# Kernel optimization log

Hardware: AMD Instinct MI355X
Metric: run time of the kernel (lower is better)

The kernel has to match this reference:

```python
import jax, jax.numpy as jnp
import numpy as np

B, C, H, W = 32, 64, 64, 64   # C == embedding_dim
K = 1024                      # num_embeddings


def setup_inputs() -> dict:
    key = jax.random.key(0)
    kx, ke = jax.random.split(key)
    x = jax.random.normal(kx, (B, C, H, W), dtype=jnp.float32)
    # codebook init in torch is uniform(-sqrt(3), sqrt(3)); any float values work for the math
    limit = 3.0 ** 0.5
    embedding = jax.random.uniform(ke, (K, C), dtype=jnp.float32, minval=-limit, maxval=limit)
    return {"x": x, "embedding": embedding}


def reference(x, embedding):
    """Eval-mode forward of Vector_Quantizer (EMA buffer updates are a
    training-only in-place side effect and are not part of the functional output)."""
    Bx, Cx, Hx, Wx = x.shape
    # [B, C, H, W] -> [B*H*W, C]
    flat_x = jnp.transpose(x, (0, 2, 3, 1)).reshape(-1, Cx)
    # squared L2 distances: ||z||^2 - 2 z.e^T + ||e||^2   -> [N, K]
    distances = (
        jnp.sum(flat_x * flat_x, axis=1, keepdims=True)
        - 2.0 * (flat_x @ embedding.T)
        + jnp.sum(embedding * embedding, axis=1)[None, :]
    )
    encoding_indices = jnp.argmin(distances, axis=1)            # [N] int
    quantized = embedding[encoding_indices]                     # [N, C] gather
    quantized = quantized.reshape(Bx, Hx, Wx, Cx).transpose(0, 3, 1, 2)  # [B,C,H,W]
    # commitment loss: 0.25 * mse(stop_grad(quantized), x)
    e_latent_loss = jnp.mean((jax.lax.stop_gradient(quantized) - x) ** 2)
    loss = 0.25 * e_latent_loss
    # straight-through estimator
    quantized_st = x + jax.lax.stop_gradient(quantized - x)
    return loss, quantized_st, encoding_indices
```

## Files before the change

kernel.cpp:

```cpp
#include <hip/hip_runtime.h>

#define NPTS   131072
#define CDIM   64
#define KCODES 1024
#define HW     4096
#define CHW    (CDIM*HW)
#define NELEM  8388608

#define FLAG_THR 2.5e-2f
#define WLCAP    32768
#define NFB_WAVES 1024

typedef __attribute__((ext_vector_type(8))) short bf16x8;
typedef __attribute__((ext_vector_type(4))) float f32x4;

#define WS_NORM_OFF 8
#define WS_EHI_OFF  (8 + KCODES)

__device__ inline unsigned short f32_to_bf16_rn(float f) {
    unsigned u = __builtin_bit_cast(unsigned, f);
    unsigned r = (u + 0x7FFFu + ((u >> 16) & 1u)) >> 16;
    return (unsigned short)r;
}
__device__ inline float bf16_to_f32(unsigned short h) {
    unsigned u = ((unsigned)h) << 16;
    return __builtin_bit_cast(float, u);
}

__global__ void vq_prep(const float* __restrict__ emb, float* __restrict__ ws) {
    int k = blockIdx.x * 256 + threadIdx.x;
    float* norms = ws + WS_NORM_OFF;
    unsigned short* ehi = (unsigned short*)(ws + WS_EHI_OFF);
    unsigned short* elo = ehi + KCODES * CDIM;
    int* wl_cnt = (int*)(elo + KCODES * CDIM);
    if (k == 0) { ws[0] = 0.0f; *wl_cnt = 0; }
    if (k < KCODES) {
        const float4* row = (const float4*)(emb + k * CDIM);
        double s = 0.0;
        #pragma unroll
        for (int c4 = 0; c4 < CDIM / 4; ++c4) {
            float4 v = row[c4];
            s += (double)v.x * v.x + (double)v.y * v.y
               + (double)v.z * v.z + (double)v.w * v.w;
            float vv[4] = {v.x, v.y, v.z, v.w};
            #pragma unroll
            for (int t = 0; t < 4; ++t) {
                unsigned short hi = f32_to_bf16_rn(vv[t]);
                float hif = bf16_to_f32(hi);
                unsigned short lo = f32_to_bf16_rn(vv[t] - hif);
                ehi[k * CDIM + c4 * 4 + t] = hi;
                elo[k * CDIM + c4 * 4 + t] = lo;
            }
        }
        norms[k] = (float)s;
    }
}

__global__ __launch_bounds__(256) void vq_main(
    const float* __restrict__ x,
    const float* __restrict__ emb,
    float* __restrict__ ws,
    float* __restrict__ out)
{
    const float* norms = ws + WS_NORM_OFF;
    const unsigned short* ehi = (const unsigned short*)(ws + WS_EHI_OFF);
    const unsigned short* elo = ehi + KCODES * CDIM;
    int* wl_cnt = (int*)(elo + KCODES * CDIM);
    int* wl = wl_cnt + 16;

    const int lane = threadIdx.x & 63;
    const int widx = threadIdx.x >> 6;
    const int wb   = (blockIdx.x * 4 + widx) * 64;
    const int lrow = lane & 15;
    const int lk   = lane >> 4;

    __shared__ int   s_idx[4][64];
    __shared__ float s_gap[4][64];

    bf16x8 ahi[4][2], alo[4][2];
    #pragma unroll
    for (int m = 0; m < 4; ++m) {
        int p = wb + m * 16 + lrow;
        const float* xb = x + (p >> 12) * CHW + (p & (HW - 1));
        #pragma unroll
        for (int h = 0; h < 2; ++h) {
            #pragma unroll
            for (int j = 0; j < 8; ++j) {
                int c = h * 32 + lk * 8 + j;
                float v = -2.0f * xb[c * HW];
                unsigned short hi = f32_to_bf16_rn(v);
                float hif = bf16_to_f32(hi);
                unsigned short lo = f32_to_bf16_rn(v - hif);
                ahi[m][h][j] = (short)hi;
                alo[m][h][j] = (short)lo;
            }
        }
    }

    float best[4][4], sec[4][4];
    int   bidx[4][4];
    #pragma unroll
    for (int m = 0; m < 4; ++m)
        #pragma unroll
        for (int r = 0; r < 4; ++r) { best[m][r] = 3.4e38f; sec[m][r] = 3.4e38f; bidx[m][r] = 0; }

    for (int n0 = 0; n0 < KCODES; n0 += 16) {
        const int code = n0 + lrow;
        const unsigned short* eh = ehi + code * CDIM + lk * 8;
        const unsigned short* el = elo + code * CDIM + lk * 8;
        bf16x8 bh0 = *(const bf16x8*)(eh);
        bf16x8 bh1 = *(const bf16x8*)(eh + 32);
        bf16x8 bl0 = *(const bf16x8*)(el);
        bf16x8 bl1 = *(const bf16x8*)(el + 32);
        float nrm = norms[code];

        f32x4 acc[4];
        #pragma unroll
        for (int m = 0; m < 4; ++m) acc[m] = (f32x4){nrm, nrm, nrm, nrm};
        #pragma unroll
        for (int m = 0; m < 4; ++m) acc[m] = __builtin_amdgcn_mfma_f32_16x16x32_bf16(ahi[m][0], bh0, acc[m], 0, 0, 0);
        #pragma unroll
        for (int m = 0; m < 4; ++m) acc[m] = __builtin_amdgcn_mfma_f32_16x16x32_bf16(ahi[m][1], bh1, acc[m], 0, 0, 0);
        #pragma unroll
        for (int m = 0; m < 4; ++m) acc[m] = __builtin_amdgcn_mfma_f32_16x16x32_bf16(alo[m][0], bh0, acc[m], 0, 0, 0);
        #pragma unroll
        for (int m = 0; m < 4; ++m) acc[m] = __builtin_amdgcn_mfma_f32_16x16x32_bf16(alo[m][1], bh1, acc[m], 0, 0, 0);
        #pragma unroll
        for (int m = 0; m < 4; ++m) acc[m] = __builtin_amdgcn_mfma_f32_16x16x32_bf16(ahi[m][0], bl0, acc[m], 0, 0, 0);
        #pragma unroll
        for (int m = 0; m < 4; ++m) acc[m] = __builtin_amdgcn_mfma_f32_16x16x32_bf16(ahi[m][1], bl1, acc[m], 0, 0, 0);

        #pragma unroll
        for (int m = 0; m < 4; ++m) {
            #pragma unroll
            for (int r = 0; r < 4; ++r) {
                float sc = acc[m][r];
                bool  lt = sc < best[m][r];
                float ns = fminf(sec[m][r], sc);
                sec[m][r]  = lt ? best[m][r] : ns;
                best[m][r] = lt ? sc : best[m][r];
                bidx[m][r] = lt ? code : bidx[m][r];
            }
        }
    }

    #pragma unroll
    for (int m = 0; m < 4; ++m) {
        #pragma unroll
        for (int r = 0; r < 4; ++r) {
            float b_ = best[m][r], s_ = sec[m][r];
            int   i_ = bidx[m][r];
            #pragma unroll
            for (int msk = 1; msk < 16; msk <<= 1) {
                float ob = __shfl_xor(b_, msk, 64);
                float os = __shfl_xor(s_, msk, 64);
                int   oi = __shfl_xor(i_, msk, 64);
                float nsec = fminf(fminf(s_, os), fmaxf(b_, ob));
                bool take = (ob < b_) || (ob == b_ && oi < i_);
                b_ = take ? ob : b_;
                i_ = take ? oi : i_;
                s_ = nsec;
            }
            if (lrow == 0) {
                int pl = m * 16 + lk * 4 + r;
                s_idx[widx][pl] = i_;
                s_gap[widx][pl] = s_ - b_;
            }
        }
    }
    __syncthreads();

    const int p = wb + lane;
    const int myidx = s_idx[widx][lane];
    const float gap = s_gap[widx][lane];
    if (gap < FLAG_THR) {
        int slot = atomicAdd(wl_cnt, 1);
        if (slot < WLCAP) wl[slot] = p;
    }
    out[1 + NELEM + p] = (float)myidx;

    const int b = p >> 12, sp = p & (HW - 1);
    const float*  xr   = x + b * CHW + sp;
    float*        orow = out + 1 + b * CHW + sp;
    const float4* er   = (const float4*)(emb + myidx * CDIM);
    float lsum = 0.0f;
    #pragma unroll
    for (int c4 = 0; c4 < CDIM / 4; ++c4) {
        float4 q = er[c4];
        float qq[4] = {q.x, q.y, q.z, q.w};
        #pragma unroll
        for (int t = 0; t < 4; ++t) {
            int c = c4 * 4 + t;
            float xv = xr[c * HW];
            float d = qq[t] - xv;
            lsum += d * d;
            orow[c * HW] = qq[t];
        }
    }
    #pragma unroll
    for (int off = 32; off > 0; off >>= 1)
        lsum += __shfl_down(lsum, off, 64);
    if (lane == 0) atomicAdd(ws, lsum);
}

__global__ __launch_bounds__(256) void vq_fallback(
    const float* __restrict__ x,
    const float* __restrict__ emb,
    float* __restrict__ ws,
    float* __restrict__ out)
{
    const unsigned short* ehi = (const unsigned short*)(ws + WS_EHI_OFF);
    const unsigned short* elo = ehi + KCODES * CDIM;
    const int* wl_cnt = (const int*)(elo + KCODES * CDIM);
    const int* wl = wl_cnt + 16;

    const int lane = threadIdx.x & 63;
    const int slot = blockIdx.x * 4 + (threadIdx.x >> 6);
    int cnt = *wl_cnt;
    if (cnt > WLCAP) cnt = WLCAP;

    for (int i = slot; i < cnt; i += NFB_WAVES) {
        const int p = wl[i];
        const int b = p >> 12, sp = p & (HW - 1);
        const float* xr = x + b * CHW + sp;
        float z[CDIM];
        #pragma unroll
        for (int c = 0; c < CDIM; ++c) z[c] = xr[c * HW];

        double bd = 1e300;
        int    bi = 0;
        for (int kk = 0; kk < 16; ++kk) {
            int k = kk * 64 + lane;
            const float4* er = (const float4*)(emb + k * CDIM);
            double s = 0.0;
            #pragma unroll
            for (int c4 = 0; c4 < CDIM / 4; ++c4) {
                float4 e = er[c4];
                double t0 = (double)z[c4 * 4 + 0] - (double)e.x;
                double t1 = (double)z[c4 * 4 + 1] - (double)e.y;
                double t2 = (double)z[c4 * 4 + 2] - (double)e.z;
                double t3 = (double)z[c4 * 4 + 3] - (double)e.w;
                s += t0 * t0 + t1 * t1 + t2 * t2 + t3 * t3;
            }
            if (s < bd) { bd = s; bi = k; }
        }
        #pragma unroll
        for (int msk = 1; msk < 64; msk <<= 1) {
            double od = __shfl_xor(bd, msk, 64);
            int    oi = __shfl_xor(bi, msk, 64);
            bool take = (od < bd) || (od == bd && oi < bi);
            bd = take ? od : bd;
            bi = take ? oi : bi;
        }
        const int oldidx = (int)out[1 + NELEM + p];
        if (bi != oldidx) {
            if (lane == 0) out[1 + NELEM + p] = (float)bi;
            float xv = xr[lane * HW];
            float qn = emb[bi * CDIM + lane];
            float qo = emb[oldidx * CDIM + lane];
            out[1 + b * CHW + lane * HW + sp] = qn;
            float dl = (qn - xv) * (qn - xv) - (qo - xv) * (qo - xv);
            #pragma unroll
            for (int off = 32; off > 0; off >>= 1)
                dl += __shfl_down(dl, off, 64);
            if (lane == 0) atomicAdd(ws, dl);
        }
    }
}

__global__ void vq_final(const float* __restrict__ ws, float* __restrict__ out) {
    if (threadIdx.x == 0 && blockIdx.x == 0)
        out[0] = 0.25f * ws[0] / (float)NELEM;
}

extern "C" void kernel_launch(void* const* d_in, const int* in_sizes, int n_in,
                              void* d_out, int out_size, void* d_ws, size_t ws_size,
                              hipStream_t stream) {
    const float* x   = (const float*)d_in[0];
    const float* emb = (const float*)d_in[1];
    float* out = (float*)d_out;
    float* ws  = (float*)d_ws;

    vq_prep<<<4, 256, 0, stream>>>(emb, ws);
    vq_main<<<NPTS / 256, 256, 0, stream>>>(x, emb, ws, out);
    vq_fallback<<<NFB_WAVES / 4, 256, 0, stream>>>(x, emb, ws, out);
    vq_final<<<1, 64, 0, stream>>>(ws, out);
}
```

Baseline: 218.5 us.

## Switch distance GEMM to fp16 split, packed integer keys, and pre-swizzled codebook

Replaces the bf16 hi/lo six-MFMA scheme with an fp16 split of scaled x (four MFMAs per tile, codebook kept in fp16 only), and packs quantised distance plus code index into a 32-bit key so min3/med3 instructions track the best and second-best candidates. The codebook is pre-laid out in MFMA-fragment order with norms, and the loads are double-buffered across code groups. Near-ties are still sent to the exact fallback through an integer-gap threshold. This cuts MFMA count and argmin ALU work, but quantising distances to integer keys and dropping the codebook low part may send more points to the fallback path.

```diff
diff --git a/kernel.cpp b/kernel.cpp
--- a/kernel.cpp
+++ b/kernel.cpp
@@ -7,65 +7,51 @@
 #define CHW    (CDIM*HW)
 #define NELEM  8388608
 
-#define FLAG_THR 2.5e-2f
-#define WLCAP    32768
-#define NFB_WAVES 1024
-
-typedef __attribute__((ext_vector_type(8))) short bf16x8;
-typedef __attribute__((ext_vector_type(4))) float f32x4;
-
-#define WS_NORM_OFF 8
-#define WS_EHI_OFF  (8 + KCODES)
-
-__device__ inline unsigned short f32_to_bf16_rn(float f) {
-    unsigned u = __builtin_bit_cast(unsigned, f);
-    unsigned r = (u + 0x7FFFu + ((u >> 16) & 1u)) >> 16;
-    return (unsigned short)r;
-}
-__device__ inline float bf16_to_f32(unsigned short h) {
-    unsigned u = ((unsigned)h) << 16;
-    return __builtin_bit_cast(float, u);
+#define NGROUP  64
+#define GSTRIDE 2304
+#define WS_BP   8
+#define WS_WL   (WS_BP + (NGROUP*GSTRIDE)/4)
+#define WLCAP   16384
+#define NFB_WAVES 2048
+#define THR_KEY (256u << 10)
+
+typedef __attribute__((ext_vector_type(8))) _Float16 f16x8;
+typedef __attribute__((ext_vector_type(4))) float    f32x4;
+
+__device__ inline unsigned umin3(unsigned a, unsigned b, unsigned c) {
+    unsigned d; asm("v_min3_u32 %0, %1, %2, %3" : "=v"(d) : "v"(a), "v"(b), "v"(c)); return d;
+}
+__device__ inline unsigned umed3(unsigned a, unsigned b, unsigned c) {
+    unsigned d; asm("v_med3_u32 %0, %1, %2, %3" : "=v"(d) : "v"(a), "v"(b), "v"(c)); return d;
 }
 
 __global__ void vq_prep(const float* __restrict__ emb, float* __restrict__ ws) {
-    int k = blockIdx.x * 256 + threadIdx.x;
-    float* norms = ws + WS_NORM_OFF;
-    unsigned short* ehi = (unsigned short*)(ws + WS_EHI_OFF);
-    unsigned short* elo = ehi + KCODES * CDIM;
-    int* wl_cnt = (int*)(elo + KCODES * CDIM);
-    if (k == 0) { ws[0] = 0.0f; *wl_cnt = 0; }
-    if (k < KCODES) {
-        const float4* row = (const float4*)(emb + k * CDIM);
-        double s = 0.0;
-        #pragma unroll
-        for (int c4 = 0; c4 < CDIM / 4; ++c4) {
-            float4 v = row[c4];
-            s += (double)v.x * v.x + (double)v.y * v.y
-               + (double)v.z * v.z + (double)v.w * v.w;
-            float vv[4] = {v.x, v.y, v.z, v.w};
-            #pragma unroll
-            for (int t = 0; t < 4; ++t) {
-                unsigned short hi = f32_to_bf16_rn(vv[t]);
-                float hif = bf16_to_f32(hi);
-                unsigned short lo = f32_to_bf16_rn(vv[t] - hif);
-                ehi[k * CDIM + c4 * 4 + t] = hi;
-                elo[k * CDIM + c4 * 4 + t] = lo;
-            }
-        }
-        norms[k] = (float)s;
-    }
-}
-
-__global__ __launch_bounds__(256) void vq_main(
-    const float* __restrict__ x,
-    const float* __restrict__ emb,
-    float* __restrict__ ws,
-    float* __restrict__ out)
+    int t = blockIdx.x * 256 + threadIdx.x;
+    if (t == 0) { ws[0] = 0.0f; ((int*)(ws + WS_WL))[0] = 0; }
+    int g = t >> 6, l = t & 63;
+    int code = g * 16 + (l & 15);
+    int ch0  = (l >> 4) * 8;
+    char* bp = (char*)(ws + WS_BP) + g * GSTRIDE;
+    const float* row = emb + code * CDIM;
+    double s = 0.0;
+    for (int c = 0; c < CDIM; ++c) { double v = row[c]; s += v * v; }
+    *(float*)(bp + 2048 + l * 4) = (float)(s * 1024.0);
+    f16x8 h0, h1;
+    #pragma unroll
+    for (int j = 0; j < 8; ++j) {
+        h0[j] = (_Float16)row[ch0 + j];
+        h1[j] = (_Float16)row[32 + ch0 + j];
+    }
+    *(f16x8*)(bp + l * 16)        = h0;
+    *(f16x8*)(bp + 1024 + l * 16) = h1;
+}
+
+__global__ __launch_bounds__(256, 2) void vq_main(
+    const float* __restrict__ x, const float* __restrict__ emb,
+    float* __restrict__ ws, float* __restrict__ out)
 {
-    const float* norms = ws + WS_NORM_OFF;
-    const unsigned short* ehi = (const unsigned short*)(ws + WS_EHI_OFF);
-    const unsigned short* elo = ehi + KCODES * CDIM;
-    int* wl_cnt = (int*)(elo + KCODES * CDIM);
+    const char* bp = (const char*)(ws + WS_BP);
+    int* wl_cnt = (int*)(ws + WS_WL);
     int* wl = wl_cnt + 16;
 
     const int lane = threadIdx.x & 63;
@@ -74,96 +60,119 @@
     const int lrow = lane & 15;
     const int lk   = lane >> 4;
 
-    __shared__ int   s_idx[4][64];
-    __shared__ float s_gap[4][64];
-
-    bf16x8 ahi[4][2], alo[4][2];
+    __shared__ int      s_idx[4][64];
+    __shared__ unsigned s_gap[4][64];
+
+    f16x8 ah[4][2], al[4][2];
+    float znorm[4];
     #pragma unroll
     for (int m = 0; m < 4; ++m) {
         int p = wb + m * 16 + lrow;
         const float* xb = x + (p >> 12) * CHW + (p & (HW - 1));
+        float zsq = 0.f;
         #pragma unroll
         for (int h = 0; h < 2; ++h) {
             #pragma unroll
             for (int j = 0; j < 8; ++j) {
                 int c = h * 32 + lk * 8 + j;
-                float v = -2.0f * xb[c * HW];
-                unsigned short hi = f32_to_bf16_rn(v);
-                float hif = bf16_to_f32(hi);
-                unsigned short lo = f32_to_bf16_rn(v - hif);
-                ahi[m][h][j] = (short)hi;
-                alo[m][h][j] = (short)lo;
-            }
-        }
-    }
-
-    float best[4][4], sec[4][4];
-    int   bidx[4][4];
+                float v = -2048.0f * xb[c * HW];
+                zsq = fmaf(v, v, zsq);
+                _Float16 hi = (_Float16)v;
+                _Float16 lo = (_Float16)(v - (float)hi);
+                ah[m][h][j] = hi; al[m][h][j] = lo;
+            }
+        }
+        zsq *= (1.0f / 4096.0f);
+        zsq += __shfl_xor(zsq, 16, 64);
+        zsq += __shfl_xor(zsq, 32, 64);
+        znorm[m] = zsq;
+    }
+    f32x4 zs[4];
     #pragma unroll
     for (int m = 0; m < 4; ++m)
         #pragma unroll
-        for (int r = 0; r < 4; ++r) { best[m][r] = 3.4e38f; sec[m][r] = 3.4e38f; bidx[m][r] = 0; }
-
-    for (int n0 = 0; n0 < KCODES; n0 += 16) {
-        const int code = n0 + lrow;
-        const unsigned short* eh = ehi + code * CDIM + lk * 8;
-        const unsigned short* el = elo + code * CDIM + lk * 8;
-        bf16x8 bh0 = *(const bf16x8*)(eh);
-        bf16x8 bh1 = *(const bf16x8*)(eh + 32);
-        bf16x8 bl0 = *(const bf16x8*)(el);
-        bf16x8 bl1 = *(const bf16x8*)(el + 32);
-        float nrm = norms[code];
-
-        f32x4 acc[4];
-        #pragma unroll
-        for (int m = 0; m < 4; ++m) acc[m] = (f32x4){nrm, nrm, nrm, nrm};
-        #pragma unroll
-        for (int m = 0; m < 4; ++m) acc[m] = __builtin_amdgcn_mfma_f32_16x16x32_bf16(ahi[m][0], bh0, acc[m], 0, 0, 0);
-        #pragma unroll
-        for (int m = 0; m < 4; ++m) acc[m] = __builtin_amdgcn_mfma_f32_16x16x32_bf16(ahi[m][1], bh1, acc[m], 0, 0, 0);
-        #pragma unroll
-        for (int m = 0; m < 4; ++m) acc[m] = __builtin_amdgcn_mfma_f32_16x16x32_bf16(alo[m][0], bh0, acc[m], 0, 0, 0);
-        #pragma unroll
-        for (int m = 0; m < 4; ++m) acc[m] = __builtin_amdgcn_mfma_f32_16x16x32_bf16(alo[m][1], bh1, acc[m], 0, 0, 0);
-        #pragma unroll
-        for (int m = 0; m < 4; ++m) acc[m] = __builtin_amdgcn_mfma_f32_16x16x32_bf16(ahi[m][0], bl0, acc[m], 0, 0, 0);
-        #pragma unroll
-        for (int m = 0; m < 4; ++m) acc[m] = __builtin_amdgcn_mfma_f32_16x16x32_bf16(ahi[m][1], bl1, acc[m], 0, 0, 0);
-
+        for (int r = 0; r < 4; ++r)
+            zs[m][r] = __shfl(znorm[m], lk * 4 + r, 64) + 512.0f;
+
+    unsigned best[4][4], sec[4][4];
+    #pragma unroll
+    for (int m = 0; m < 4; ++m)
+        #pragma unroll
+        for (int r = 0; r < 4; ++r) { best[m][r] = 0xFFFFFFFFu; sec[m][r] = 0xFFFFFFFFu; }
+
+    f16x8 b0A, b1A, b2A, b3A, b0B, b1B, b2B, b3B;
+    float n0A, n1A, n0B, n1B;
+
+    auto LOADP = [&](int p, f16x8& v0, f16x8& v1, f16x8& v2, f16x8& v3, float& m0, float& m1) {
+        const char* g0 = bp + (2 * p) * GSTRIDE;
+        const char* g1 = g0 + GSTRIDE;
+        v0 = *(const f16x8*)(g0 + lane * 16);
+        v1 = *(const f16x8*)(g0 + 1024 + lane * 16);
+        v2 = *(const f16x8*)(g1 + lane * 16);
+        v3 = *(const f16x8*)(g1 + 1024 + lane * 16);
+        m0 = *(const float*)(g0 + 2048 + lane * 4);
+        m1 = *(const float*)(g1 + 2048 + lane * 4);
+    };
+    auto COMP = [&](int p, const f16x8& v0, const f16x8& v1, const f16x8& v2, const f16x8& v3,
+                    float m0, float m1) {
+        f32x4 a0[4], a1[4];
+        #pragma unroll
+        for (int m = 0; m < 4; ++m) a0[m] = __builtin_amdgcn_mfma_f32_16x16x32_f16(ah[m][0], v0, zs[m], 0, 0, 0);
+        #pragma unroll
+        for (int m = 0; m < 4; ++m) a0[m] = __builtin_amdgcn_mfma_f32_16x16x32_f16(ah[m][1], v1, a0[m], 0, 0, 0);
+        #pragma unroll
+        for (int m = 0; m < 4; ++m) a0[m] = __builtin_amdgcn_mfma_f32_16x16x32_f16(al[m][0], v0, a0[m], 0, 0, 0);
+        #pragma unroll
+        for (int m = 0; m < 4; ++m) a0[m] = __builtin_amdgcn_mfma_f32_16x16x32_f16(al[m][1], v1, a0[m], 0, 0, 0);
+        #pragma unroll
+        for (int m = 0; m < 4; ++m) a1[m] = __builtin_amdgcn_mfma_f32_16x16x32_f16(ah[m][0], v2, zs[m], 0, 0, 0);
+        #pragma unroll
+        for (int m = 0; m < 4; ++m) a1[m] = __builtin_amdgcn_mfma_f32_16x16x32_f16(ah[m][1], v3, a1[m], 0, 0, 0);
+        #pragma unroll
+        for (int m = 0; m < 4; ++m) a1[m] = __builtin_amdgcn_mfma_f32_16x16x32_f16(al[m][0], v2, a1[m], 0, 0, 0);
+        #pragma unroll
+        for (int m = 0; m < 4; ++m) a1[m] = __builtin_amdgcn_mfma_f32_16x16x32_f16(al[m][1], v3, a1[m], 0, 0, 0);
+
+        unsigned code0 = (unsigned)(2 * p * 16) | (unsigned)lrow;
+        unsigned code1 = code0 + 16u;
         #pragma unroll
         for (int m = 0; m < 4; ++m) {
             #pragma unroll
             for (int r = 0; r < 4; ++r) {
-                float sc = acc[m][r];
-                bool  lt = sc < best[m][r];
-                float ns = fminf(sec[m][r], sc);
-                sec[m][r]  = lt ? best[m][r] : ns;
-                best[m][r] = lt ? sc : best[m][r];
-                bidx[m][r] = lt ? code : bidx[m][r];
-            }
-        }
+                float d0 = a0[m][r] + m0;
+                float d1 = a1[m][r] + m1;
+                unsigned u0 = ((unsigned)d0 << 10) | code0;
+                unsigned u1 = ((unsigned)d1 << 10) | code1;
+                unsigned md = umed3(best[m][r], u0, u1);
+                best[m][r] = umin3(best[m][r], u0, u1);
+                sec[m][r]  = min(sec[m][r], md);
+            }
+        }
+    };
+
+    LOADP(0, b0A, b1A, b2A, b3A, n0A, n1A);
+    for (int it = 0; it < 16; ++it) {
+        LOADP(2 * it + 1, b0B, b1B, b2B, b3B, n0B, n1B);
+        COMP(2 * it, b0A, b1A, b2A, b3A, n0A, n1A);
+        LOADP((2 * it + 2) & 31, b0A, b1A, b2A, b3A, n0A, n1A);
+        COMP(2 * it + 1, b0B, b1B, b2B, b3B, n0B, n1B);
     }
 
     #pragma unroll
     for (int m = 0; m < 4; ++m) {
         #pragma unroll
         for (int r = 0; r < 4; ++r) {
-            float b_ = best[m][r], s_ = sec[m][r];
-            int   i_ = bidx[m][r];
+            unsigned b_ = best[m][r], s_ = sec[m][r];
             #pragma unroll
             for (int msk = 1; msk < 16; msk <<= 1) {
-                float ob = __shfl_xor(b_, msk, 64);
-                float os = __shfl_xor(s_, msk, 64);
-                int   oi = __shfl_xor(i_, msk, 64);
-                float nsec = fminf(fminf(s_, os), fmaxf(b_, ob));
-                bool take = (ob < b_) || (ob == b_ && oi < i_);
-                b_ = take ? ob : b_;
-                i_ = take ? oi : i_;
-                s_ = nsec;
+                unsigned ob = (unsigned)__shfl_xor((int)b_, msk, 64);
+                unsigned os = (unsigned)__shfl_xor((int)s_, msk, 64);
+                s_ = min(min(s_, os), max(b_, ob));
+                b_ = min(b_, ob);
             }
             if (lrow == 0) {
                 int pl = m * 16 + lk * 4 + r;
-                s_idx[widx][pl] = i_;
+                s_idx[widx][pl] = (int)(b_ & 1023u);
                 s_gap[widx][pl] = s_ - b_;
             }
         }
@@ -172,8 +181,7 @@
 
     const int p = wb + lane;
     const int myidx = s_idx[widx][lane];
-    const float gap = s_gap[widx][lane];
-    if (gap < FLAG_THR) {
+    if (s_gap[widx][lane] < THR_KEY) {
         int slot = atomicAdd(wl_cnt, 1);
         if (slot < WLCAP) wl[slot] = p;
     }
@@ -183,7 +191,7 @@
     const float*  xr   = x + b * CHW + sp;
     float*        orow = out + 1 + b * CHW + sp;
     const float4* er   = (const float4*)(emb + myidx * CDIM);
-    float lsum = 0.0f;
+    float lsum = 0.f;
     #pragma unroll
     for (int c4 = 0; c4 < CDIM / 4; ++c4) {
         float4 q = er[c4];
@@ -204,16 +212,11 @@
 }
 
 __global__ __launch_bounds__(256) void vq_fallback(
-    const float* __restrict__ x,
-    const float* __restrict__ emb,
-    float* __restrict__ ws,
-    float* __restrict__ out)
+    const float* __restrict__ x, const float* __restrict__ emb,
+    float* __restrict__ ws, float* __restrict__ out)
 {
-    const unsigned short* ehi = (const unsigned short*)(ws + WS_EHI_OFF);
-    const unsigned short* elo = ehi + KCODES * CDIM;
-    const int* wl_cnt = (const int*)(elo + KCODES * CDIM);
+    const int* wl_cnt = (const int*)(ws + WS_WL);
     const int* wl = wl_cnt + 16;
-
     const int lane = threadIdx.x & 63;
     const int slot = blockIdx.x * 4 + (threadIdx.x >> 6);
     int cnt = *wl_cnt;
@@ -281,7 +284,7 @@
     float* out = (float*)d_out;
     float* ws  = (float*)d_ws;
 
-    vq_prep<<<4, 256, 0, stream>>>(emb, ws);
+    vq_prep<<<16, 256, 0, stream>>>(emb, ws);
     vq_main<<<NPTS / 256, 256, 0, stream>>>(x, emb, ws, out);
     vq_fallback<<<NFB_WAVES / 4, 256, 0, stream>>>(x, emb, ws, out);
     vq_final<<<1, 64, 0, stream>>>(ws, out);
```

Measured after the change: 374.2 us. 71.3% more time.
